# Optimization experiments

Hardware: AMD Instinct MI355X
Metric: run time of the kernel (lower is better)

Reference implementation:

```python
import jax, jax.numpy as jnp
import numpy as np

B, T, C = 2, 1024, 2048
H, N = 32, 64
D_DECAY = 96; D_AAA = 96; D_MV = 64; D_GATE = 256
EPS_GN = 1e-5 * 64.0  # eps * head_size_divisor**2, divisor=8


def setup_inputs() -> dict:
    key = jax.random.key(0)
    ks = jax.random.split(key, 24)
    rn = lambda k, s, sc=1.0: jax.random.normal(k, s, jnp.float32) * sc
    ru = lambda k, s: jax.random.uniform(k, s, jnp.float32)
    sw = C ** -0.5
    return dict(
        x=rn(ks[0], (B, T, C)),
        v_first=rn(ks[1], (B, T, C)),
        shift_state=rn(ks[2], (B, C)),
        wkv_state=jnp.zeros((B, H, N, N), jnp.float32),
        x_r=ru(ks[3], (1, 1, C)), x_w=ru(ks[4], (1, 1, C)), x_k=ru(ks[5], (1, 1, C)),
        x_v=ru(ks[6], (1, 1, C)), x_a=ru(ks[7], (1, 1, C)), x_g=ru(ks[8], (1, 1, C)),
        w0=jnp.linspace(-7.0, -2.0, C, dtype=jnp.float32).reshape(1, 1, C) + 0.5,
        w1=rn(ks[9], (C, D_DECAY), sw), w2=rn(ks[10], (D_DECAY, C), 0.1 * D_DECAY ** -0.5),
        a0=jnp.zeros((1, 1, C), jnp.float32),
        a1=rn(ks[11], (C, D_AAA), sw), a2=rn(ks[12], (D_AAA, C), 0.1 * D_AAA ** -0.5),
        v0=jnp.ones((1, 1, C), jnp.float32),
        v1=rn(ks[13], (C, D_MV), sw), v2=rn(ks[14], (D_MV, C), 0.1 * D_MV ** -0.5),
        g1=rn(ks[15], (C, D_GATE), sw), g2=rn(ks[16], (D_GATE, C), 0.1 * D_GATE ** -0.5),
        k_k=0.85 * jnp.ones((1, 1, C), jnp.float32),
        k_a=jnp.ones((1, 1, C), jnp.float32),
        r_k=rn(ks[17], (H, N), 0.1),
        W_r=rn(ks[18], (C, C), sw), W_k=rn(ks[19], (C, C), sw),
        W_v=rn(ks[20], (C, C), sw), W_o=rn(ks[21], (C, C), sw),
        gn_w=jnp.ones((C,), jnp.float32), gn_b=jnp.zeros((C,), jnp.float32),
    )


def _forward(x, v_first, shift_state, wkv_state, x_r, x_w, x_k, x_v, x_a, x_g,
             w0, w1, w2, a0, a1, a2, v0, v1, v2, g1, g2, k_k, k_a, r_k,
             W_r, W_k, W_v, W_o, gn_w, gn_b):
    # token shift (ZeroPad2d((0,0,1,-1)) == prepend shift_state, drop last)
    xx = jnp.concatenate([shift_state[:, None, :], x[:, :-1]], axis=1) - x
    xr = x + xx * x_r; xw = x + xx * x_w; xk = x + xx * x_k
    xv = x + xx * x_v; xa = x + xx * x_a; xg = x + xx * x_g
    r = xr @ W_r.T
    w = -jax.nn.softplus(-(w0 + jnp.tanh(xw @ w1) @ w2)) - 0.5  # <= -0.5
    k = xk @ W_k.T
    v = xv @ W_v.T
    v = v + (v_first - v) * jax.nn.sigmoid(v0 + (xv @ v1) @ v2)  # layer_id != 0
    a = jax.nn.sigmoid(a0 + (xa @ a1) @ a2)
    g = jax.nn.sigmoid(xg @ g1) @ g2
    kk = (k * k_k).reshape(B, T, H, N)
    kk = kk / jnp.maximum(jnp.linalg.norm(kk, axis=-1, keepdims=True), 1e-12)  # F.normalize
    k = k * (1.0 + (a - 1.0) * k_a)
    # RWKV-7 recurrence: S_t = S * diag(exp(-exp(w))) + (S a) b^T + v k^T ; o_t = S r
    wdec = jnp.exp(-jnp.exp(w))                           # [B,T,C] in (0,1)
    tm = lambda z: z.reshape(B, T, H, N).transpose(1, 0, 2, 3)  # -> [T,B,H,N]
    xs = (tm(r), tm(wdec), tm(k), tm(v),
          -kk.transpose(1, 0, 2, 3),
          (kk * a.reshape(B, T, H, N)).transpose(1, 0, 2, 3))

    def step(S, ins):  # S: [B,H,N_v,N_k]
        rr, ww, kc, vv, aa, bb = ins
        Sa = jnp.einsum('bhvk,bhk->bhv', S, aa)
        S = S * ww[:, :, None, :] + Sa[..., None] * bb[:, :, None, :] + vv[..., None] * kc[:, :, None, :]
        return S, jnp.einsum('bhvk,bhk->bhv', S, rr)

    S_f, o = jax.lax.scan(step, wkv_state, xs)
    o = o.transpose(1, 0, 2, 3)                           # [B,T,H,N]
    # GroupNorm(H, C): per-(B*T) sample, normalize each head's N channels
    mu = o.mean(-1, keepdims=True)
    var = o.var(-1, keepdims=True)
    o = (o - mu) * jax.lax.rsqrt(var + EPS_GN) * gn_w.reshape(H, N) + gn_b.reshape(H, N)
    rh = r.reshape(B, T, H, N); kh = k.reshape(B, T, H, N); vh = v.reshape(B, T, H, N)
    o = o + (rh * kh * r_k).sum(-1, keepdims=True) * vh
    out = (o.reshape(B, T, C) * g) @ W_o.T
    return out, S_f


def reference(x, v_first, shift_state, wkv_state, x_r, x_w, x_k, x_v, x_a, x_g,
              w0, w1, w2, a0, a1, a2, v0, v1, v2, g1, g2, k_k, k_a, r_k,
              W_r, W_k, W_v, W_o, gn_w, gn_b):
    out, S_f = _forward(x, v_first, shift_state, wkv_state, x_r, x_w, x_k, x_v, x_a, x_g,
                        w0, w1, w2, a0, a1, a2, v0, v1, v2, g1, g2, k_k, k_a, r_k,
                        W_r, W_k, W_v, W_o, gn_w, gn_b)
    return (out, S_f)
```

## Files before the change

### kernel.cpp

```cpp
#include <hip/hip_runtime.h>
#include <stdint.h>

typedef __attribute__((ext_vector_type(4))) float f32x4;
typedef __attribute__((ext_vector_type(8))) __bf16 bf16x8;

#define DEVINL __device__ __forceinline__

constexpr int T_LEN = 1024;
constexpr int CDIM  = 2048;
constexpr int MROWS = 2048;
constexpr size_t MC = (size_t)MROWS * CDIM;

constexpr size_t SZ_BF  = MC * 2;
constexpr size_t SZ_F32 = MC * 4;
constexpr size_t oXr  = 0;
constexpr size_t oXw  = oXr + SZ_BF;
constexpr size_t oXk  = oXw + SZ_BF;
constexpr size_t oXv  = oXk + SZ_BF;
constexpr size_t oXa  = oXv + SZ_BF;
constexpr size_t oXg  = oXa + SZ_BF;
constexpr size_t oWr  = oXg + SZ_BF;
constexpr size_t oWk  = oWr + SZ_BF;
constexpr size_t oWv  = oWk + SZ_BF;
constexpr size_t oWo  = oWv + SZ_BF;
constexpr size_t oW1T = oWo + SZ_BF;
constexpr size_t oA1T = oW1T + 524288;
constexpr size_t oV1T = oA1T + 524288;
constexpr size_t oG1T = oV1T + 524288;
constexpr size_t oW2T = oG1T + 1048576;
constexpr size_t oA2T = oW2T + 524288;
constexpr size_t oV2T = oA2T + 524288;
constexpr size_t oG2T = oV2T + 524288;
constexpr size_t oHw  = oG2T + 1048576;
constexpr size_t oHa  = oHw + 524288;
constexpr size_t oHv  = oHa + 524288;
constexpr size_t oHg  = oHv + 524288;
constexpr size_t oR   = oHg + 1048576;
constexpr size_t oK   = oR  + SZ_F32;
constexpr size_t oV   = oK  + SZ_F32;
constexpr size_t oWW  = oV  + SZ_F32;
constexpr size_t oAA  = oWW + SZ_F32;
constexpr size_t oBB  = oAA + SZ_F32;
constexpr size_t oG   = oBB + SZ_F32;
constexpr size_t oO   = oG  + SZ_F32;
constexpr size_t oAout= oO  + SZ_F32;

DEVINL unsigned short f2bf(float f) {
  uint32_t u = __builtin_bit_cast(uint32_t, f);
  u += 0x7fffu + ((u >> 16) & 1u);
  return (unsigned short)(u >> 16);
}
DEVINL void st_bf4(unsigned short* p, f32x4 v) {
  ushort4 o;
  o.x = f2bf(v[0]); o.y = f2bf(v[1]); o.z = f2bf(v[2]); o.w = f2bf(v[3]);
  *(ushort4*)p = o;
}
DEVINL void gload16(const void* g, void* l) {
  __builtin_amdgcn_global_load_lds(
      (const __attribute__((address_space(1))) unsigned int*)g,
      (__attribute__((address_space(3))) unsigned int*)l, 16, 0, 0);
}

template <int CTL>
DEVINL float redrot(float x) {
  int y = __builtin_amdgcn_update_dpp(0, __builtin_bit_cast(int, x),
                                      CTL, 0xF, 0xF, true);
  return x + __builtin_bit_cast(float, y);
}
DEVINL float redrow16(float x) {
  x = redrot<0x128>(x); x = redrot<0x124>(x);
  x = redrot<0x122>(x); x = redrot<0x121>(x);
  return x;
}
#if __has_builtin(__builtin_amdgcn_permlane16_swap)
DEVINL float red16(float x, bool evenrow) {
  unsigned xi = __builtin_bit_cast(unsigned, x);
  auto r = __builtin_amdgcn_permlane16_swap(xi, xi, false, false);
  unsigned oth = evenrow ? (unsigned)r[1] : (unsigned)r[0];
  return x + __builtin_bit_cast(float, oth);
}
#else
DEVINL float red16(float x, bool) { return x + __shfl_xor(x, 16); }
#endif
#if __has_builtin(__builtin_amdgcn_permlane32_swap)
DEVINL float red32(float x, bool lowhalf) {
  unsigned xi = __builtin_bit_cast(unsigned, x);
  auto r = __builtin_amdgcn_permlane32_swap(xi, xi, false, false);
  unsigned oth = lowhalf ? (unsigned)r[1] : (unsigned)r[0];
  return x + __builtin_bit_cast(float, oth);
}
#else
DEVINL float red32(float x, bool) { return x + __shfl_xor(x, 32); }
#endif

struct Conv4 { const float* s0; const float* s1; const float* s2; const float* s3;
               unsigned short* d0; unsigned short* d1; unsigned short* d2; unsigned short* d3; };
__global__ void k_conv4(Conv4 c, int n4) {
  int i = blockIdx.x * 256 + threadIdx.x;
  if (i >= n4) return;
  const float* s = (blockIdx.y == 0) ? c.s0 : (blockIdx.y == 1) ? c.s1
                   : (blockIdx.y == 2) ? c.s2 : c.s3;
  unsigned short* d = (blockIdx.y == 0) ? c.d0 : (blockIdx.y == 1) ? c.d1
                      : (blockIdx.y == 2) ? c.d2 : c.d3;
  f32x4 v = *(const f32x4*)(s + (size_t)i * 4);
  st_bf4(d + (size_t)i * 4, v);
}

struct TpJobs {
  const float* src[8];
  unsigned short* dst[8];
  int sR[8]; int sC[8]; int dR[8]; int dC[8];
};
__global__ void k_tp8(TpJobs jt) {
  const int j = blockIdx.y;
  const int n = jt.dR[j] * jt.dC[j];
  int i = blockIdx.x * 256 + threadIdx.x;
  if (i >= n) return;
  const int dC = jt.dC[j], sR = jt.sR[j], sC = jt.sC[j];
  int r = i / dC, c = i - r * dC;
  float v = (r < sC && c < sR) ? jt.src[j][(size_t)c * sC + r] : 0.f;
  jt.dst[j][i] = f2bf(v);
}

__global__ void k_mix(const float* __restrict__ x, const float* __restrict__ shift,
                      const float* __restrict__ cr, const float* __restrict__ cw,
                      const float* __restrict__ ck, const float* __restrict__ cv,
                      const float* __restrict__ ca, const float* __restrict__ cg,
                      unsigned short* __restrict__ Xr, unsigned short* __restrict__ Xw,
                      unsigned short* __restrict__ Xk, unsigned short* __restrict__ Xv,
                      unsigned short* __restrict__ Xa, unsigned short* __restrict__ Xg) {
  int i = blockIdx.x * 256 + threadIdx.x;
  size_t e = (size_t)i * 4;
  int m = (int)(e >> 11);
  int c = (int)(e & 2047);
  int t = m & (T_LEN - 1);
  int b = m >> 10;
  f32x4 xc = *(const f32x4*)(x + e);
  f32x4 pv = (t == 0) ? *(const f32x4*)(shift + (size_t)b * CDIM + c)
                      : *(const f32x4*)(x + e - CDIM);
  f32x4 xx = pv - xc;
  st_bf4(Xr + e, xc + xx * (*(const f32x4*)(cr + c)));
  st_bf4(Xw + e, xc + xx * (*(const f32x4*)(cw + c)));
  st_bf4(Xk + e, xc + xx * (*(const f32x4*)(ck + c)));
  st_bf4(Xv + e, xc + xx * (*(const f32x4*)(cv + c)));
  st_bf4(Xa + e, xc + xx * (*(const f32x4*)(ca + c)));
  st_bf4(Xg + e, xc + xx * (*(const f32x4*)(cg + c)));
}

struct GemmJob { const unsigned short* A; const unsigned short* B; void* C;
                 int epi; int ldc; int n; int K; };
struct GemmBatch { GemmJob j[8]; };

__global__ __launch_bounds__(256) void k_gemm_nt(GemmBatch gb) {
  const GemmJob jb = gb.j[blockIdx.z];
  const int K = jb.K;
  const int gx = gridDim.x;
  const int nwg = gx * gridDim.y;
  const int fid = blockIdx.y * gx + blockIdx.x;
  const int swz = (fid & 7) * (nwg >> 3) + (fid >> 3);
  const int rowB = (swz / gx) * 128;
  const int colB = (swz % gx) * 128;
  if (colB >= jb.n) return;
  const int ldc = jb.ldc;
  __shared__ __align__(16) unsigned short As[128 * 32];
  __shared__ __align__(16) unsigned short Bs[128 * 32];
  const int tid  = threadIdx.x;
  const int lane = tid & 63;
  const int wv   = tid >> 6;
  const int wm = wv >> 1, wn = wv & 1;
  const size_t rsb = (size_t)K * 2;
  const int c0 = wv, c1 = wv + 4;
  const char* Ag0 = (const char*)jb.A + (size_t)(rowB + c0 * 16 + (lane >> 2)) * rsb + (lane & 3) * 16;
  const char* Ag1 = (const char*)jb.A + (size_t)(rowB + c1 * 16 + (lane >> 2)) * rsb + (lane & 3) * 16;
  const char* Bg0 = (const char*)jb.B + (size_t)(colB + c0 * 16 + (lane >> 2)) * rsb + (lane & 3) * 16;
  const char* Bg1 = (const char*)jb.B + (size_t)(colB + c1 * 16 + (lane >> 2)) * rsb + (lane & 3) * 16;
  unsigned short* Al0 = As + c0 * 512;
  unsigned short* Al1 = As + c1 * 512;
  unsigned short* Bl0 = Bs + c0 * 512;
  unsigned short* Bl1 = Bs + c1 * 512;
  f32x4 acc[4][4];
#pragma unroll
  for (int mi = 0; mi < 4; ++mi)
#pragma unroll
    for (int ni = 0; ni < 4; ++ni) acc[mi][ni] = (f32x4){0.f, 0.f, 0.f, 0.f};
  const int KT = K >> 5;
  const int fr = lane & 15, fk = (lane >> 4) * 8;
  for (int kt = 0; kt < KT; ++kt) {
    __syncthreads();
    gload16(Ag0, Al0); gload16(Ag1, Al1);
    gload16(Bg0, Bl0); gload16(Bg1, Bl1);
    Ag0 += 64; Ag1 += 64; Bg0 += 64; Bg1 += 64;
    __syncthreads();
    bf16x8 af[4], bfv[4];
#pragma unroll
    for (int mi = 0; mi < 4; ++mi)
      af[mi] = *(const bf16x8*)&As[(wm * 64 + mi * 16 + fr) * 32 + fk];
#pragma unroll
    for (int ni = 0; ni < 4; ++ni)
      bfv[ni] = *(const bf16x8*)&Bs[(wn * 64 + ni * 16 + fr) * 32 + fk];
#pragma unroll
    for (int mi = 0; mi < 4; ++mi)
#pragma unroll
      for (int ni = 0; ni < 4; ++ni)
        acc[mi][ni] = __builtin_amdgcn_mfma_f32_16x16x32_bf16(af[mi], bfv[ni], acc[mi][ni], 0, 0, 0);
  }
  const int er = (lane >> 4) * 4, ec = lane & 15;
  if (jb.epi == 0) {
    float* Cf = (float*)jb.C;
#pragma unroll
    for (int mi = 0; mi < 4; ++mi)
#pragma unroll
      for (int ni = 0; ni < 4; ++ni) {
        int row0 = rowB + wm * 64 + mi * 16 + er;
        int col  = colB + wn * 64 + ni * 16 + ec;
#pragma unroll
        for (int j = 0; j < 4; ++j)
          Cf[(size_t)(row0 + j) * ldc + col] = acc[mi][ni][j];
      }
  } else {
    unsigned short* Cb = (unsigned short*)jb.C;
#pragma unroll
    for (int mi = 0; mi < 4; ++mi)
#pragma unroll
      for (int ni = 0; ni < 4; ++ni) {
        int row0 = rowB + wm * 64 + mi * 16 + er;
        int col  = colB + wn * 64 + ni * 16 + ec;
#pragma unroll
        for (int j = 0; j < 4; ++j) {
          float val = acc[mi][ni][j];
          if (jb.epi == 2) val = tanhf(val);
          else if (jb.epi == 3) val = 1.f / (1.f + __expf(-val));
          Cb[(size_t)(row0 + j) * ldc + col] = f2bf(val);
        }
      }
  }
}

__global__ __launch_bounds__(256) void k_post(
    float* __restrict__ Kb, float* __restrict__ Vb, float* __restrict__ Wb,
    float* __restrict__ Ab, float* __restrict__ Bb,
    const float* __restrict__ vf, const float* __restrict__ w0,
    const float* __restrict__ a0, const float* __restrict__ v0,
    const float* __restrict__ kkc, const float* __restrict__ kac) {
  const int wv = threadIdx.x >> 6, lane = threadIdx.x & 63;
  const int gw = blockIdx.x * 4 + wv;
  const int m = gw >> 3, q = gw & 7;
  const int c = q * 256 + lane * 4;
  const size_t idx = (size_t)m * CDIM + c;
  f32x4 kraw = *(const f32x4*)(Kb + idx);
  f32x4 vraw = *(const f32x4*)(Vb + idx);
  f32x4 wlr  = *(const f32x4*)(Wb + idx);
  f32x4 alr  = *(const f32x4*)(Ab + idx);
  f32x4 vlr  = *(const f32x4*)(Bb + idx);
  f32x4 vf4  = *(const f32x4*)(vf + idx);
  f32x4 w04  = *(const f32x4*)(w0 + c);
  f32x4 a04  = *(const f32x4*)(a0 + c);
  f32x4 v04  = *(const f32x4*)(v0 + c);
  f32x4 kkc4 = *(const f32x4*)(kkc + c);
  f32x4 kac4 = *(const f32x4*)(kac + c);
  f32x4 wdec, aa, vv, kk, kn;
#pragma unroll
  for (int j = 0; j < 4; ++j) {
    float z = w04[j] + wlr[j];
    float sg = 1.f / (1.f + __expf(-z));
    wdec[j] = __expf(-0.60653065971f * sg);
    aa[j] = 1.f / (1.f + __expf(-(a04[j] + alr[j])));
    float vgate = 1.f / (1.f + __expf(-(v04[j] + vlr[j])));
    vv[j] = vraw[j] + (vf4[j] - vraw[j]) * vgate;
    kk[j] = kraw[j] * kkc4[j];
    kn[j] = kraw[j] * (1.f + (aa[j] - 1.f) * kac4[j]);
  }
  float s2 = kk[0] * kk[0] + kk[1] * kk[1] + kk[2] * kk[2] + kk[3] * kk[3];
  s2 = redrow16(s2);
  float inv = 1.f / fmaxf(sqrtf(s2), 1e-12f);
  f32x4 nkk = kk * inv;
  *(f32x4*)(Wb + idx) = wdec;
  *(f32x4*)(Vb + idx) = vv;
  *(f32x4*)(Kb + idx) = kn;
  *(f32x4*)(Ab + idx) = -nkk;
  *(f32x4*)(Bb + idx) = nkk * aa;
}

__global__ __launch_bounds__(64) void k_scan(
    const float* __restrict__ Rb, const float* __restrict__ Wb,
    const float* __restrict__ Kb, const float* __restrict__ Vb,
    const float* __restrict__ Ab, const float* __restrict__ Bb,
    const float* __restrict__ S0, float* __restrict__ Ob,
    float* __restrict__ Sf) {
  const int bid = blockIdx.x;
  const int bh = bid & 63, vo = bid >> 6;
  const int b = bh >> 5, h = bh & 31;
  const int lane = threadIdx.x;
  const int vr = lane & 3;
  const int kq = lane >> 2;
  const int gv = vo * 4 + vr;
  const int kk0 = kq * 4;
  const bool evr = ((lane >> 4) & 1) == 0;
  const bool lhf = lane < 32;
  __shared__ __align__(16) float stg[4][6][64];
  const size_t rowBase = (size_t)b * T_LEN * CDIM;
  const size_t colBase = (size_t)h * 64;
  const float* pR = Rb + rowBase + colBase + lane;
  const float* pW = Wb + rowBase + colBase + lane;
  const float* pK = Kb + rowBase + colBase + lane;
  const float* pV = Vb + rowBase + colBase + lane;
  const float* pA = Ab + rowBase + colBase + lane;
  const float* pB = Bb + rowBase + colBase + lane;
  float* Obp = Ob + rowBase + colBase + vo * 4 + lane;
  f32x4 s0;
  {
    const float* sp = S0 + (((size_t)(b * 32 + h)) * 64 + gv) * 64 + kk0;
    s0 = *(const f32x4*)sp;
  }
  float gA[6], gB[6];
  {
    float h0[6], h1[6];
    h0[0] = pR[0]; h0[1] = pW[0]; h0[2] = pK[0]; h0[3] = pV[0]; h0[4] = pA[0]; h0[5] = pB[0];
    h1[0] = pR[CDIM]; h1[1] = pW[CDIM]; h1[2] = pK[CDIM]; h1[3] = pV[CDIM]; h1[4] = pA[CDIM]; h1[5] = pB[CDIM];
#pragma unroll
    for (int j = 0; j < 6; ++j) { stg[0][j][lane] = h0[j]; stg[1][j][lane] = h1[j]; }
    gA[0] = pR[2 * CDIM]; gA[1] = pW[2 * CDIM]; gA[2] = pK[2 * CDIM];
    gA[3] = pV[2 * CDIM]; gA[4] = pA[2 * CDIM]; gA[5] = pB[2 * CDIM];
    gB[0] = pR[3 * CDIM]; gB[1] = pW[3 * CDIM]; gB[2] = pK[3 * CDIM];
    gB[3] = pV[3 * CDIM]; gB[4] = pA[3 * CDIM]; gB[5] = pB[3 * CDIM];
  }
  f32x4 aR, aW, aK, aA, aB; float aVV;
  f32x4 bR, bW, bK, bA, bB; float bVV;
  aR = *(const f32x4*)&stg[0][0][kk0];
  aW = *(const f32x4*)&stg[0][1][kk0];
  aK = *(const f32x4*)&stg[0][2][kk0];
  aA = *(const f32x4*)&stg[0][4][kk0];
  aB = *(const f32x4*)&stg[0][5][kk0];
  aVV = stg[0][3][gv];
  float pox = 0.f;
#define SCAN_STEP(T, G, SR,SW,SK,SA,SB,SVV, NR,NW,NK,NA,NB,NVV, FIRST) do {    \
    f32x4 _sv = SA * s0;                                                       \
    float _sa = _sv[0] + _sv[1] + _sv[2] + _sv[3];                             \
    { const int _np = ((T) + 1) & 3;          \
      NR = *(const f32x4*)&stg[_np][0][kk0];                                   \
      NW = *(const f32x4*)&stg[_np][1][kk0];                                   \
      NK = *(const f32x4*)&stg[_np][2][kk0];                                   \
      NA = *(const f32x4*)&stg[_np][4][kk0];                                   \
      NB = *(const f32x4*)&stg[_np][5][kk0];                                   \
      NVV = stg[_np][3][gv]; }                                                 \
    float _po = pox;                                                           \
    _sa = redrot<0x124>(_sa); _po = redrot<0x124>(_po);                        \
    _sa = redrot<0x128>(_sa); _po = redrot<0x128>(_po);                        \
    _sa = red16(_sa, evr);    _po = red16(_po, evr);                           \
    _sa = red32(_sa, lhf);    _po = red32(_po, lhf);                           \
    if (!(FIRST) && lane < 4) Obp[(size_t)((T) - 1) * CDIM] = _po;             \
    { const int _ws = ((T) + 2) & 3;                                           \
      stg[_ws][0][lane] = G[0]; stg[_ws][1][lane] = G[1];                      \
      stg[_ws][2][lane] = G[2]; stg[_ws][3][lane] = G[3];                      \
      stg[_ws][4][lane] = G[4]; stg[_ws][5][lane] = G[5];                      \
      const size_t _to = (size_t)(((T) + 4 < T_LEN) ? (T) + 4 : T_LEN - 1) * CDIM; \
      G[0] = pR[_to]; G[1] = pW[_to]; G[2] = pK[_to];                          \
      G[3] = pV[_to]; G[4] = pA[_to]; G[5] = pB[_to]; }                        \
    s0 = s0 * SW + _sa * SB + SVV * SK;                                        \
    f32x4 _ov = s0 * SR;                                                       \
    pox = _ov[0] + _ov[1] + _ov[2] + _ov[3];                                   \
  } while (0)
#define SCAN_STEP_I(...) SCAN_STEP(__VA_ARGS__)
#define ASET aR,aW,aK,aA,aB,aVV
#define BSET bR,bW,bK,bA,bB,bVV
  SCAN_STEP_I(0, gA, ASET, BSET, true);
  SCAN_STEP_I(1, gB, BSET, ASET, false);
  for (int t = 2; t < T_LEN; t += 2) {
    SCAN_STEP_I(t, gA, ASET, BSET, false);
    SCAN_STEP_I(t + 1, gB, BSET, ASET, false);
  }
#undef SCAN_STEP
#undef SCAN_STEP_I
#undef ASET
#undef BSET
  {
    float _po = pox;
    _po = redrot<0x124>(_po);
    _po = redrot<0x128>(_po);
    _po = red16(_po, evr);
    _po = red32(_po, lhf);
    if (lane < 4) Obp[(size_t)(T_LEN - 1) * CDIM] = _po;
  }
  float* sfp = Sf + (((size_t)(b * 32 + h)) * 64 + gv) * 64 + kk0;
  *(f32x4*)sfp = s0;
}

__global__ __launch_bounds__(256) void k_gn(
    const float* __restrict__ Ob, const float* __restrict__ Rb,
    const float* __restrict__ Kb, const float* __restrict__ Vb,
    const float* __restrict__ Gb, const float* __restrict__ rk,
    const float* __restrict__ gw, const float* __restrict__ gb2,
    unsigned short* __restrict__ Aout) {
  const int wv = threadIdx.x >> 6, lane = threadIdx.x & 63;
  const int gwv = blockIdx.x * 4 + wv;
  const int m = gwv >> 3, q = gwv & 7;
  const int c = q * 256 + lane * 4;
  const size_t idx = (size_t)m * CDIM + c;
  f32x4 o  = *(const f32x4*)(Ob + idx);
  f32x4 r  = *(const f32x4*)(Rb + idx);
  f32x4 k  = *(const f32x4*)(Kb + idx);
  f32x4 v  = *(const f32x4*)(Vb + idx);
  f32x4 g  = *(const f32x4*)(Gb + idx);
  f32x4 rk4 = *(const f32x4*)(rk + c);
  f32x4 gw4 = *(const f32x4*)(gw + c);
  f32x4 gb4 = *(const f32x4*)(gb2 + c);
  float t1 = o[0] + o[1] + o[2] + o[3];
  float t2 = o[0]*o[0] + o[1]*o[1] + o[2]*o[2] + o[3]*o[3];
  f32x4 rkv = r * k * rk4;
  float t3 = rkv[0] + rkv[1] + rkv[2] + rkv[3];
  t1 = redrow16(t1);
  t2 = redrow16(t2);
  t3 = redrow16(t3);
  float mean = t1 * (1.f / 64.f);
  float var = t2 * (1.f / 64.f) - mean * mean;
  float rstd = rsqrtf(var + 6.4e-4f);
  f32x4 og = (o - mean) * rstd * gw4 + gb4 + t3 * v;
  st_bf4(Aout + idx, og * g);
}

extern "C" void kernel_launch(void* const* d_in, const int* in_sizes, int n_in,
                              void* d_out, int out_size, void* d_ws, size_t ws_size,
                              hipStream_t stream) {
  (void)in_sizes; (void)n_in; (void)out_size; (void)ws_size;
  const float* x      = (const float*)d_in[0];
  const float* vfirst = (const float*)d_in[1];
  const float* shift  = (const float*)d_in[2];
  const float* wkv0   = (const float*)d_in[3];
  const float* xr_c   = (const float*)d_in[4];
  const float* xw_c   = (const float*)d_in[5];
  const float* xk_c   = (const float*)d_in[6];
  const float* xv_c   = (const float*)d_in[7];
  const float* xa_c   = (const float*)d_in[8];
  const float* xg_c   = (const float*)d_in[9];
  const float* w0     = (const float*)d_in[10];
  const float* w1     = (const float*)d_in[11];
  const float* w2     = (const float*)d_in[12];
  const float* a0     = (const float*)d_in[13];
  const float* a1     = (const float*)d_in[14];
  const float* a2     = (const float*)d_in[15];
  const float* v0     = (const float*)d_in[16];
  const float* v1     = (const float*)d_in[17];
  const float* v2     = (const float*)d_in[18];
  const float* g1     = (const float*)d_in[19];
  const float* g2     = (const float*)d_in[20];
  const float* k_k    = (const float*)d_in[21];
  const float* k_a    = (const float*)d_in[22];
  const float* r_k    = (const float*)d_in[23];
  const float* W_r    = (const float*)d_in[24];
  const float* W_k    = (const float*)d_in[25];
  const float* W_v    = (const float*)d_in[26];
  const float* W_o    = (const float*)d_in[27];
  const float* gn_w   = (const float*)d_in[28];
  const float* gn_b   = (const float*)d_in[29];
  char* ws = (char*)d_ws;
  auto BF = [&](size_t o) { return (unsigned short*)(ws + o); };
  auto FP = [&](size_t o) { return (float*)(ws + o); };

  { Conv4 cb{W_r, W_k, W_v, W_o, BF(oWr), BF(oWk), BF(oWv), BF(oWo)};
    k_conv4<<<dim3(4096, 4), 256, 0, stream>>>(cb, 1048576); }
  { TpJobs jt{};
    jt.src[0] = w1; jt.dst[0] = BF(oW1T); jt.sR[0] = 2048; jt.sC[0] = 96;   jt.dR[0] = 128;  jt.dC[0] = 2048;
    jt.src[1] = a1; jt.dst[1] = BF(oA1T); jt.sR[1] = 2048; jt.sC[1] = 96;   jt.dR[1] = 128;  jt.dC[1] = 2048;
    jt.src[2] = v1; jt.dst[2] = BF(oV1T); jt.sR[2] = 2048; jt.sC[2] = 64;   jt.dR[2] = 128;  jt.dC[2] = 2048;
    jt.src[3] = g1; jt.dst[3] = BF(oG1T); jt.sR[3] = 2048; jt.sC[3] = 256;  jt.dR[3] = 256;  jt.dC[3] = 2048;
    jt.src[4] = w2; jt.dst[4] = BF(oW2T); jt.sR[4] = 96;   jt.sC[4] = 2048; jt.dR[4] = 2048; jt.dC[4] = 128;
    jt.src[5] = a2; jt.dst[5] = BF(oA2T); jt.sR[5] = 96;   jt.sC[5] = 2048; jt.dR[5] = 2048; jt.dC[5] = 128;
    jt.src[6] = v2; jt.dst[6] = BF(oV2T); jt.sR[6] = 64;   jt.sC[6] = 2048; jt.dR[6] = 2048; jt.dC[6] = 128;
    jt.src[7] = g2; jt.dst[7] = BF(oG2T); jt.sR[7] = 256;  jt.sC[7] = 2048; jt.dR[7] = 2048; jt.dC[7] = 256;
    k_tp8<<<dim3(2048, 8), 256, 0, stream>>>(jt); }
  k_mix<<<4096, 256, 0, stream>>>(x, shift, xr_c, xw_c, xk_c, xv_c, xa_c, xg_c,
                                  BF(oXr), BF(oXw), BF(oXk), BF(oXv), BF(oXa), BF(oXg));
  { GemmBatch gb{};
    gb.j[0] = {BF(oXr), BF(oWr),  FP(oR),  0, 2048, 2048, 2048};
    gb.j[1] = {BF(oXk), BF(oWk),  FP(oK),  0, 2048, 2048, 2048};
    gb.j[2] = {BF(oXv), BF(oWv),  FP(oV),  0, 2048, 2048, 2048};
    gb.j[3] = {BF(oXw), BF(oW1T), BF(oHw), 2, 128, 128, 2048};
    gb.j[4] = {BF(oXa), BF(oA1T), BF(oHa), 1, 128, 128, 2048};
    gb.j[5] = {BF(oXv), BF(oV1T), BF(oHv), 1, 128, 128, 2048};
    gb.j[6] = {BF(oXg), BF(oG1T), BF(oHg), 3, 256, 256, 2048};
    k_gemm_nt<<<dim3(16, 16, 7), 256, 0, stream>>>(gb); }
  { GemmBatch gb{};
    gb.j[0] = {BF(oHw), BF(oW2T), FP(oWW), 0, 2048, 2048, 128};
    gb.j[1] = {BF(oHa), BF(oA2T), FP(oAA), 0, 2048, 2048, 128};
    gb.j[2] = {BF(oHv), BF(oV2T), FP(oBB), 0, 2048, 2048, 128};
    gb.j[3] = {BF(oHg), BF(oG2T), FP(oG),  0, 2048, 2048, 256};
    k_gemm_nt<<<dim3(16, 16, 4), 256, 0, stream>>>(gb); }
  k_post<<<4096, 256, 0, stream>>>(FP(oK), FP(oV), FP(oWW), FP(oAA), FP(oBB),
                                   vfirst, w0, a0, v0, k_k, k_a);
  k_scan<<<1024, 64, 0, stream>>>(FP(oR), FP(oWW), FP(oK), FP(oV), FP(oAA), FP(oBB),
                                  wkv0, FP(oO), (float*)d_out + MC);
  k_gn<<<4096, 256, 0, stream>>>(FP(oO), FP(oR), FP(oK), FP(oV), FP(oG),
                                 r_k, gn_w, gn_b, BF(oAout));
  { GemmBatch gb{};
    gb.j[0] = {BF(oAout), BF(oWo), d_out, 0, 2048, 2048, 2048};
    k_gemm_nt<<<dim3(16, 16, 1), 256, 0, stream>>>(gb); }
}
```

Before: 568.7 us.

## Split-K the output projection GEMM and widen token-mix vectorization

The final output projection GEMM is split along K into two halves run as a batched launch, writing partial sums into reused fp32 scratch buffers; a new elementwise kernel then adds them into the output. This doubles the workgroup count for the single 256-tile GEMM so more compute units are busy, at the cost of an extra full fp32 write/read pass and a kernel launch. The GEMM job struct gains separate leading dimensions for A and B to support this. Separately, the token-mix kernel now processes 8 elements per thread instead of 4, halving its grid.

```diff
diff --git a/kernel.cpp b/kernel.cpp
--- a/kernel.cpp
+++ b/kernel.cpp
@@ -130,25 +130,33 @@
                       unsigned short* __restrict__ Xk, unsigned short* __restrict__ Xv,
                       unsigned short* __restrict__ Xa, unsigned short* __restrict__ Xg) {
   int i = blockIdx.x * 256 + threadIdx.x;
-  size_t e = (size_t)i * 4;
+  size_t e = (size_t)i * 8;
   int m = (int)(e >> 11);
   int c = (int)(e & 2047);
   int t = m & (T_LEN - 1);
   int b = m >> 10;
-  f32x4 xc = *(const f32x4*)(x + e);
-  f32x4 pv = (t == 0) ? *(const f32x4*)(shift + (size_t)b * CDIM + c)
-                      : *(const f32x4*)(x + e - CDIM);
-  f32x4 xx = pv - xc;
-  st_bf4(Xr + e, xc + xx * (*(const f32x4*)(cr + c)));
-  st_bf4(Xw + e, xc + xx * (*(const f32x4*)(cw + c)));
-  st_bf4(Xk + e, xc + xx * (*(const f32x4*)(ck + c)));
-  st_bf4(Xv + e, xc + xx * (*(const f32x4*)(cv + c)));
-  st_bf4(Xa + e, xc + xx * (*(const f32x4*)(ca + c)));
-  st_bf4(Xg + e, xc + xx * (*(const f32x4*)(cg + c)));
+  f32x4 xc0 = *(const f32x4*)(x + e);
+  f32x4 xc1 = *(const f32x4*)(x + e + 4);
+  f32x4 pv0, pv1;
+  if (t == 0) {
+    pv0 = *(const f32x4*)(shift + (size_t)b * CDIM + c);
+    pv1 = *(const f32x4*)(shift + (size_t)b * CDIM + c + 4);
+  } else {
+    pv0 = *(const f32x4*)(x + e - CDIM);
+    pv1 = *(const f32x4*)(x + e - CDIM + 4);
+  }
+  f32x4 xx0 = pv0 - xc0, xx1 = pv1 - xc1;
+#define MIX1(P, CF) do {                                                       \
+    st_bf4(P + e,     xc0 + xx0 * (*(const f32x4*)(CF + c)));                  \
+    st_bf4(P + e + 4, xc1 + xx1 * (*(const f32x4*)(CF + c + 4)));              \
+  } while (0)
+  MIX1(Xr, cr); MIX1(Xw, cw); MIX1(Xk, ck);
+  MIX1(Xv, cv); MIX1(Xa, ca); MIX1(Xg, cg);
+#undef MIX1
 }
 
 struct GemmJob { const unsigned short* A; const unsigned short* B; void* C;
-                 int epi; int ldc; int n; int K; };
+                 int epi; int ldc; int n; int K; int lda; int ldb; };
 struct GemmBatch { GemmJob j[8]; };
 
 __global__ __launch_bounds__(256) void k_gemm_nt(GemmBatch gb) {
@@ -168,10 +176,11 @@
   const int lane = tid & 63;
   const int wv   = tid >> 6;
   const int wm = wv >> 1, wn = wv & 1;
-  const size_t rsb = (size_t)K * 2;
+  const size_t rsa = (size_t)jb.lda * 2;
+  const size_t rsb = (size_t)jb.ldb * 2;
   const int c0 = wv, c1 = wv + 4;
-  const char* Ag0 = (const char*)jb.A + (size_t)(rowB + c0 * 16 + (lane >> 2)) * rsb + (lane & 3) * 16;
-  const char* Ag1 = (const char*)jb.A + (size_t)(rowB + c1 * 16 + (lane >> 2)) * rsb + (lane & 3) * 16;
+  const char* Ag0 = (const char*)jb.A + (size_t)(rowB + c0 * 16 + (lane >> 2)) * rsa + (lane & 3) * 16;
+  const char* Ag1 = (const char*)jb.A + (size_t)(rowB + c1 * 16 + (lane >> 2)) * rsa + (lane & 3) * 16;
   const char* Bg0 = (const char*)jb.B + (size_t)(colB + c0 * 16 + (lane >> 2)) * rsb + (lane & 3) * 16;
   const char* Bg1 = (const char*)jb.B + (size_t)(colB + c1 * 16 + (lane >> 2)) * rsb + (lane & 3) * 16;
   unsigned short* Al0 = As + c0 * 512;
@@ -234,6 +243,15 @@
         }
       }
   }
+}
+
+__global__ void k_add(const float* __restrict__ p0, const float* __restrict__ p1,
+                      float* __restrict__ out) {
+  int i = blockIdx.x * 256 + threadIdx.x;
+  f32x4 a = *(const f32x4*)(p0 + (size_t)i * 4);
+  f32x4 b = *(const f32x4*)(p1 + (size_t)i * 4);
+  f32x4 s = a + b;
+  *(f32x4*)(out + (size_t)i * 4) = s;
 }
 
 __global__ __launch_bounds__(256) void k_post(
@@ -468,22 +486,22 @@
     jt.src[6] = v2; jt.dst[6] = BF(oV2T); jt.sR[6] = 64;   jt.sC[6] = 2048; jt.dR[6] = 2048; jt.dC[6] = 128;
     jt.src[7] = g2; jt.dst[7] = BF(oG2T); jt.sR[7] = 256;  jt.sC[7] = 2048; jt.dR[7] = 2048; jt.dC[7] = 256;
     k_tp8<<<dim3(2048, 8), 256, 0, stream>>>(jt); }
-  k_mix<<<4096, 256, 0, stream>>>(x, shift, xr_c, xw_c, xk_c, xv_c, xa_c, xg_c,
+  k_mix<<<2048, 256, 0, stream>>>(x, shift, xr_c, xw_c, xk_c, xv_c, xa_c, xg_c,
                                   BF(oXr), BF(oXw), BF(oXk), BF(oXv), BF(oXa), BF(oXg));
   { GemmBatch gb{};
-    gb.j[0] = {BF(oXr), BF(oWr),  FP(oR),  0, 2048, 2048, 2048};
-    gb.j[1] = {BF(oXk), BF(oWk),  FP(oK),  0, 2048, 2048, 2048};
-    gb.j[2] = {BF(oXv), BF(oWv),  FP(oV),  0, 2048, 2048, 2048};
-    gb.j[3] = {BF(oXw), BF(oW1T), BF(oHw), 2, 128, 128, 2048};
-    gb.j[4] = {BF(oXa), BF(oA1T), BF(oHa), 1, 128, 128, 2048};
-    gb.j[5] = {BF(oXv), BF(oV1T), BF(oHv), 1, 128, 128, 2048};
-    gb.j[6] = {BF(oXg), BF(oG1T), BF(oHg), 3, 256, 256, 2048};
+    gb.j[0] = {BF(oXr), BF(oWr),  FP(oR),  0, 2048, 2048, 2048, 2048, 2048};
+    gb.j[1] = {BF(oXk), BF(oWk),  FP(oK),  0, 2048, 2048, 2048, 2048, 2048};
+    gb.j[2] = {BF(oXv), BF(oWv),  FP(oV),  0, 2048, 2048, 2048, 2048, 2048};
+    gb.j[3] = {BF(oXw), BF(oW1T), BF(oHw), 2, 128, 128, 2048, 2048, 2048};
+    gb.j[4] = {BF(oXa), BF(oA1T), BF(oHa), 1, 128, 128, 2048, 2048, 2048};
+    gb.j[5] = {BF(oXv), BF(oV1T), BF(oHv), 1, 128, 128, 2048, 2048, 2048};
+    gb.j[6] = {BF(oXg), BF(oG1T), BF(oHg), 3, 256, 256, 2048, 2048, 2048};
     k_gemm_nt<<<dim3(16, 16, 7), 256, 0, stream>>>(gb); }
   { GemmBatch gb{};
-    gb.j[0] = {BF(oHw), BF(oW2T), FP(oWW), 0, 2048, 2048, 128};
-    gb.j[1] = {BF(oHa), BF(oA2T), FP(oAA), 0, 2048, 2048, 128};
-    gb.j[2] = {BF(oHv), BF(oV2T), FP(oBB), 0, 2048, 2048, 128};
-    gb.j[3] = {BF(oHg), BF(oG2T), FP(oG),  0, 2048, 2048, 256};
+    gb.j[0] = {BF(oHw), BF(oW2T), FP(oWW), 0, 2048, 2048, 128, 128, 128};
+    gb.j[1] = {BF(oHa), BF(oA2T), FP(oAA), 0, 2048, 2048, 128, 128, 128};
+    gb.j[2] = {BF(oHv), BF(oV2T), FP(oBB), 0, 2048, 2048, 128, 128, 128};
+    gb.j[3] = {BF(oHg), BF(oG2T), FP(oG),  0, 2048, 2048, 256, 256, 256};
     k_gemm_nt<<<dim3(16, 16, 4), 256, 0, stream>>>(gb); }
   k_post<<<4096, 256, 0, stream>>>(FP(oK), FP(oV), FP(oWW), FP(oAA), FP(oBB),
                                    vfirst, w0, a0, v0, k_k, k_a);
@@ -492,6 +510,8 @@
   k_gn<<<4096, 256, 0, stream>>>(FP(oO), FP(oR), FP(oK), FP(oV), FP(oG),
                                  r_k, gn_w, gn_b, BF(oAout));
   { GemmBatch gb{};
-    gb.j[0] = {BF(oAout), BF(oWo), d_out, 0, 2048, 2048, 2048};
-    k_gemm_nt<<<dim3(16, 16, 1), 256, 0, stream>>>(gb); }
-}
+    gb.j[0] = {BF(oAout),        BF(oWo),        FP(oWW), 0, 2048, 2048, 1024, 2048, 2048};
+    gb.j[1] = {BF(oAout) + 1024, BF(oWo) + 1024, FP(oAA), 0, 2048, 2048, 1024, 2048, 2048};
+    k_gemm_nt<<<dim3(16, 16, 2), 256, 0, stream>>>(gb); }
+  k_add<<<4096, 256, 0, stream>>>(FP(oWW), FP(oAA), (float*)d_out);
+}
```

Result: no change. 562.4 us (-1.1%).
